# Kernel tuning notes

Hardware: AMD Instinct MI355X
Metric: run time of the kernel (lower is better)

Reference implementation:

```python
import jax, jax.numpy as jnp
import numpy as np

HEAD_DIM = 64
AGGR = 4  # attn_aggr_ratio
BN_EPS = 1e-5


def _conv1x1(x, W, b=None):
    # x: [N, Cin, L], W: [Cout, Cin] -> [N, Cout, L]
    y = jnp.einsum('ncl,oc->nol', x, W)
    if b is not None:
        y = y + b[None, :, None]
    return y


def _bn(x, gamma, beta, mean, var):
    # BatchNorm1d, eval mode (running stats). x: [N, C, L]
    inv = gamma * jax.lax.rsqrt(var + BN_EPS)
    return x * inv[None, :, None] + (beta - mean * inv)[None, :, None]


def setup_inputs() -> dict:
    key = jax.random.key(0)
    ks = jax.random.split(key, 8)
    N, C, L = 4, 256, 4096
    s = 1.0 / np.sqrt(C)
    inp = {
        'x': jax.random.normal(ks[0], (N, C, L), jnp.float32),
        'Wq': jax.random.normal(ks[1], (C, C), jnp.float32) * s,
        'bq': jnp.zeros((C,), jnp.float32),
        'Wk': jax.random.normal(ks[2], (C, C), jnp.float32) * s,
        'bk': jnp.zeros((C,), jnp.float32),
        'Wv': jax.random.normal(ks[3], (C, C), jnp.float32) * s,
        'bv': jnp.zeros((C,), jnp.float32),
        'Wo': jax.random.normal(ks[4], (C, C), jnp.float32) * s,
        'bo': jnp.zeros((C,), jnp.float32),
        'Wa': jax.random.normal(ks[5], (C, C), jnp.float32) * s,
        'g1': jnp.ones((C,), jnp.float32), 'b1': jnp.zeros((C,), jnp.float32),
        'm1': jnp.zeros((C,), jnp.float32), 'v1': jnp.ones((C,), jnp.float32),
        'g2': jnp.ones((C,), jnp.float32), 'b2': jnp.zeros((C,), jnp.float32),
        'm2': jnp.zeros((C,), jnp.float32), 'v2': jnp.ones((C,), jnp.float32),
    }
    return inp


def reference(x, Wq, bq, Wk, bk, Wv, bv, Wo, bo, Wa,
              g1, b1, m1, v1, g2, b2, m2, v2):
    N, C, L = x.shape
    H, E = C // HEAD_DIM, HEAD_DIM
    # q projection on full-resolution input
    q = _conv1x1(x, Wq, bq).reshape(N, H, E, L)
    # LocalAwareAggregationBlock: avg+max pool (kernel=AGGR, L divisible), 1x1 conv, BN
    xp = x.reshape(N, C, L // AGGR, AGGR)
    xa = xp.mean(axis=-1) + xp.max(axis=-1)          # [N, C, L//AGGR]
    xa = _conv1x1(xa, Wa)                             # bias=False
    xa = _bn(xa, g1, b1, m1, v1)
    # post-aggregation norm
    xa = _bn(xa, g2, b2, m2, v2)
    k = _conv1x1(xa, Wk, bk).reshape(N, H, E, -1)     # [N, H, E, L2]
    v = _conv1x1(xa, Wv, bv).reshape(N, H, E, -1)
    # attention: softmax((q/sqrt(E))^T k) @ v^T
    scale = 1.0 / np.sqrt(E)
    scores = jnp.einsum('nhel,nhem->nhlm', q * scale, k)  # [N, H, L, L2]
    attn = jax.nn.softmax(scores, axis=-1)
    o = jnp.einsum('nhlm,nhem->nhel', attn, v).reshape(N, C, L)
    return _conv1x1(o, Wo, bo)
```

## Files before the change

kernel.cpp:

```cpp
#include <hip/hip_runtime.h>
#include <stdint.h>

constexpr int NBATCH = 4;
constexpr int CH     = 256;
constexpr int LEN    = 4096;
constexpr int LPOOL  = 1024;
constexpr int NH     = 4;
constexpr int HD     = 64;

typedef __attribute__((ext_vector_type(8))) short short8;
typedef __attribute__((ext_vector_type(4))) float float4e;

__device__ __forceinline__ unsigned short f2bf(float f) {
    union { unsigned int i; float f; } v; v.f = f;
    unsigned int lsb = (v.i >> 16) & 1u;
    v.i += 0x7fffu + lsb;
    return (unsigned short)(v.i >> 16);
}
__device__ __forceinline__ unsigned pack2bf(float lo, float hi) {
    unsigned a = __float_as_uint(lo) + 0x8000u;
    unsigned b = __float_as_uint(hi) + 0x8000u;
    return __builtin_amdgcn_perm(b, a, 0x07060302u);
}

__global__ __launch_bounds__(256) void transpool_setup(
    const float* __restrict__ x, unsigned short* __restrict__ xbf,
    unsigned short* __restrict__ poolT,
    const float* __restrict__ w0, const float* __restrict__ w1,
    const float* __restrict__ w2, const float* __restrict__ w3,
    const float* __restrict__ w4, unsigned short* __restrict__ outW,
    const float* __restrict__ g1, const float* __restrict__ b1,
    const float* __restrict__ m1, const float* __restrict__ v1,
    const float* __restrict__ g2, const float* __restrict__ b2,
    const float* __restrict__ m2, const float* __restrict__ v2,
    float* __restrict__ scale, float* __restrict__ shift,
    const float* __restrict__ bk, const float* __restrict__ bv,
    float* __restrict__ bkv)
{
    __shared__ float T[64][65];
    __shared__ float P16[64][17];
    int b = blockIdx.x, t = threadIdx.x;
    if (b >= 1024) {
        int sb = b - 1024;
        if (sb < 320) {
            int gid = sb * 256 + t;
            int w = gid >> 14;
            int off = (gid & 16383) * 4;
            const float* src = (w == 0) ? w0 : (w == 1) ? w1 : (w == 2) ? w2 : (w == 3) ? w3 : w4;
            float4 v = *(const float4*)(src + off);
            uint2 pk;
            pk.x = pack2bf(v.x, v.y);
            pk.y = pack2bf(v.z, v.w);
            *(uint2*)(outW + w * 65536 + off) = pk;
        } else {
            float inv1 = g1[t] * rsqrtf(v1[t] + 1e-5f);
            float inv2 = g2[t] * rsqrtf(v2[t] + 1e-5f);
            scale[t] = inv1 * inv2;
            shift[t] = (b1[t] - m1[t] * inv1) * inv2 + (b2[t] - m2[t] * inv2);
            bkv[t] = bk[t];
            bkv[256 + t] = bv[t];
        }
        return;
    }
    int n = b >> 8, c0 = ((b >> 6) & 3) * 64, l0 = (b & 63) * 64;
    const float* xp = x + ((size_t)n * CH + c0) * LEN + l0;
    #pragma unroll
    for (int i = 0; i < 4; i++) {
        int idx = t + i * 256;
        int c = idx >> 4, l4 = idx & 15;
        float4 v = *(const float4*)(xp + (size_t)c * LEN + l4 * 4);
        T[c][l4 * 4 + 0] = v.x; T[c][l4 * 4 + 1] = v.y;
        T[c][l4 * 4 + 2] = v.z; T[c][l4 * 4 + 3] = v.w;
        P16[c][l4] = (v.x + v.y + v.z + v.w) * 0.25f
                   + fmaxf(fmaxf(v.x, v.y), fmaxf(v.z, v.w));
    }
    __syncthreads();
    unsigned short* op = xbf + ((size_t)n * LEN + l0) * CH + c0;
    #pragma unroll
    for (int i = 0; i < 4; i++) {
        int idx = t + i * 256;
        int l = idx >> 4, c4 = idx & 15;
        uint2 pk;
        pk.x = pack2bf(T[c4 * 4 + 0][l], T[c4 * 4 + 1][l]);
        pk.y = pack2bf(T[c4 * 4 + 2][l], T[c4 * 4 + 3][l]);
        *(uint2*)(op + (size_t)l * CH + c4 * 4) = pk;
    }
    int p0 = l0 >> 2;
    #pragma unroll
    for (int k = 0; k < 2; k++) {
        int p = (t >> 5) + k * 8;
        int c2 = (t & 31) * 2;
        unsigned pk = pack2bf(P16[c2][p], P16[c2 + 1][p]);
        *(unsigned*)(poolT + ((size_t)n * LPOOL + p0 + p) * CH + c0 + c2) = pk;
    }
}

__global__ __launch_bounds__(256) void gemm_mfma(
    const unsigned short* __restrict__ A,
    const unsigned short* __restrict__ B, size_t bBatch,
    const float* __restrict__ biasRow,
    const float* __restrict__ scale, const float* __restrict__ shift,
    float* __restrict__ outF, size_t oFBatch,
    unsigned short* __restrict__ out1, size_t o1Batch, int cs1,
    unsigned short* __restrict__ out2, size_t o2Batch, int rs2, int rowSplit,
    int NN, float outScale)
{
    __shared__ unsigned short smem[2 * 128 * 72];
    unsigned short* As = smem;
    unsigned short* Bs = smem + 128 * 72;

    int n = blockIdx.z;
    int t = threadIdx.x;
    int wave = t >> 6, lane = t & 63, m = lane & 15, quad = lane >> 4;
    int wm = wave & 1, wn = wave >> 1;
    int rowTile = blockIdx.y * 128;
    int col0 = blockIdx.x * 128;

    const unsigned short* Ab = A + (size_t)rowTile * 256;
    const unsigned short* Bb = B + (size_t)n * bBatch + (size_t)col0 * 256;

    float4e acc[4][4] = {};

    for (int kk = 0; kk < 256; kk += 64) {
        #pragma unroll
        for (int i = 0; i < 4; i++) {
            int idx = t + i * 256;
            int row = idx >> 3, ch = idx & 7;
            *(uint4*)&As[row * 72 + ch * 8] = *(const uint4*)(Ab + (size_t)row * 256 + kk + ch * 8);
            *(uint4*)&Bs[row * 72 + ch * 8] = *(const uint4*)(Bb + (size_t)row * 256 + kk + ch * 8);
        }
        __syncthreads();
        #pragma unroll
        for (int kc = 0; kc < 2; kc++) {
            short8 af[4], bfr[4];
            #pragma unroll
            for (int i = 0; i < 4; i++)
                af[i] = *(const short8*)&As[(wm * 64 + i * 16 + m) * 72 + kc * 32 + quad * 8];
            #pragma unroll
            for (int j = 0; j < 4; j++)
                bfr[j] = *(const short8*)&Bs[(wn * 64 + j * 16 + m) * 72 + kc * 32 + quad * 8];
            #pragma unroll
            for (int i = 0; i < 4; i++)
                #pragma unroll
                for (int j = 0; j < 4; j++)
                    acc[i][j] = __builtin_amdgcn_mfma_f32_16x16x32_bf16(af[i], bfr[j], acc[i][j], 0, 0, 0);
        }
        __syncthreads();
    }

    if (outF) {
        float* TOf = (float*)smem;
        float* dst = outF + (size_t)n * oFBatch;
        #pragma unroll
        for (int half = 0; half < 2; half++) {
            __syncthreads();
            if (wm == half) {
                #pragma unroll
                for (int i = 0; i < 4; i++) {
                    int rowL = i * 16 + quad * 4;
                    int rowG = rowTile + half * 64 + rowL;
                    float br[4], sc[4], sh[4];
                    #pragma unroll
                    for (int r = 0; r < 4; r++) {
                        br[r] = biasRow ? biasRow[rowG + r] : 0.0f;
                        sc[r] = scale ? scale[rowG + r] : 1.0f;
                        sh[r] = shift ? shift[rowG + r] : 0.0f;
                    }
                    #pragma unroll
                    for (int j = 0; j < 4; j++) {
                        int colL = wn * 64 + j * 16 + m;
                        float4e c = acc[i][j];
                        #pragma unroll
                        for (int r = 0; r < 4; r++)
                            TOf[(rowL + r) * 128 + colL] = ((c[r] + br[r]) * sc[r] + sh[r]) * outScale;
                    }
                }
            }
            __syncthreads();
            #pragma unroll
            for (int w = 0; w < 8; w++) {
                int idx = t + w * 256;
                int row = idx >> 5, c4 = idx & 31;
                *(float4*)(dst + (size_t)(rowTile + half * 64 + row) * NN + col0 + c4 * 4) =
                    *(const float4*)&TOf[row * 128 + c4 * 4];
            }
        }
        return;
    }

    bool mode2 = (rowTile >= rowSplit);
    unsigned short* TO = smem;
    #pragma unroll
    for (int i = 0; i < 4; i++) {
        int rowL = wm * 64 + i * 16 + quad * 4;
        int rowG = rowTile + rowL;
        float br[4], sc[4], sh[4];
        #pragma unroll
        for (int r = 0; r < 4; r++) {
            br[r] = biasRow ? biasRow[rowG + r] : 0.0f;
            sc[r] = scale ? scale[rowG + r] : 1.0f;
            sh[r] = shift ? shift[rowG + r] : 0.0f;
        }
        #pragma unroll
        for (int j = 0; j < 4; j++) {
            int colL = wn * 64 + j * 16 + m;
            float4e c = acc[i][j];
            float v0 = ((c[0] + br[0]) * sc[0] + sh[0]) * outScale;
            float v1 = ((c[1] + br[1]) * sc[1] + sh[1]) * outScale;
            float v2 = ((c[2] + br[2]) * sc[2] + sh[2]) * outScale;
            float v3 = ((c[3] + br[3]) * sc[3] + sh[3]) * outScale;
            if (!mode2) {
                uint2 pk;
                pk.x = pack2bf(v0, v1);
                pk.y = pack2bf(v2, v3);
                *(uint2*)&TO[colL * 136 + rowL] = pk;
            } else {
                TO[(rowL + 0) * 136 + colL] = f2bf(v0);
                TO[(rowL + 1) * 136 + colL] = f2bf(v1);
                TO[(rowL + 2) * 136 + colL] = f2bf(v2);
                TO[(rowL + 3) * 136 + colL] = f2bf(v3);
            }
        }
    }
    __syncthreads();
    if (!mode2) {
        unsigned short* dst = out1 + (size_t)n * o1Batch;
        #pragma unroll
        for (int w = 0; w < 8; w++) {
            int idx = t + w * 256;
            int l = idx >> 4, ch = idx & 15;
            *(uint4*)(dst + (size_t)(col0 + l) * cs1 + rowTile + ch * 8) =
                *(const uint4*)&TO[l * 136 + ch * 8];
        }
    } else {
        unsigned short* dst = out2 + (size_t)n * o2Batch;
        int rowBase = rowTile - rowSplit;
        #pragma unroll
        for (int w = 0; w < 8; w++) {
            int idx = t + w * 256;
            int row = idx >> 4, ch = idx & 15;
            *(uint4*)(dst + (size_t)(rowBase + row) * rs2 + col0 + ch * 8) =
                *(const uint4*)&TO[row * 136 + ch * 8];
        }
    }
}

__global__ __launch_bounds__(256, 4) void attn_mfma(
    const unsigned short* __restrict__ Qb,
    const unsigned short* __restrict__ Kb,
    const unsigned short* __restrict__ Vb,
    unsigned short* __restrict__ Obf)
{
    __shared__ unsigned short Ks[2][64 * 72];
    __shared__ unsigned short Vs[2][64 * 72];

    int qb = blockIdx.x;
    int h  = blockIdx.y;
    int n  = blockIdx.z;
    int t  = threadIdx.x;
    int wave = t >> 6, lane = t & 63;
    int m = lane & 15, quad = lane >> 4;
    int l0 = qb * 64 + wave * 16;

    const unsigned short* qp = Qb + ((size_t)n * LEN + l0 + m) * CH + h * HD + quad * 8;
    short8 bQ[2];
    bQ[0] = *(const short8*)qp;
    bQ[1] = *(const short8*)(qp + 32);

    float4e Oa[4] = {};
    float l_run = 0.0f;

    const unsigned short* KgBase = Kb + (size_t)n * LPOOL * CH + h * HD;
    const unsigned short* VgBase = Vb + ((size_t)n * CH + h * HD) * LPOOL;
    const float NEG = -17.312340f;

    int srow[2], sch[2];
    #pragma unroll
    for (int i = 0; i < 2; i++) {
        int idx = t + i * 256;
        srow[i] = idx >> 3; sch[i] = idx & 7;
    }

    uint4 kreg[2], vreg[2];
    #pragma unroll
    for (int i = 0; i < 2; i++) {
        kreg[i] = *(const uint4*)(KgBase + (size_t)srow[i] * CH + sch[i] * 8);
        vreg[i] = *(const uint4*)(VgBase + (size_t)srow[i] * LPOOL + sch[i] * 8);
    }
    #pragma unroll
    for (int i = 0; i < 2; i++) {
        *(uint4*)&Ks[0][srow[i] * 72 + sch[i] * 8] = kreg[i];
        *(uint4*)&Vs[0][srow[i] * 72 + sch[i] * 8] = vreg[i];
    }
    __syncthreads();

    for (int kt = 0; kt < 16; kt++) {
        int cur = kt & 1;
        if (kt < 15) {
            const unsigned short* Kg2 = KgBase + (size_t)(kt + 1) * 64 * CH;
            const unsigned short* Vg2 = VgBase + (kt + 1) * 64;
            #pragma unroll
            for (int i = 0; i < 2; i++) {
                kreg[i] = *(const uint4*)(Kg2 + (size_t)srow[i] * CH + sch[i] * 8);
                vreg[i] = *(const uint4*)(Vg2 + (size_t)srow[i] * LPOOL + sch[i] * 8);
            }
        }

        #pragma unroll
        for (int ch2 = 0; ch2 < 2; ch2++) {
            const unsigned short* kpE = &Ks[cur][(ch2 * 32 + m) * 72 + quad * 8];
            const unsigned short* kpO = kpE + 16 * 72;
            short8 aE0 = *(const short8*)kpE;
            short8 aE1 = *(const short8*)(kpE + 32);
            short8 aO0 = *(const short8*)kpO;
            short8 aO1 = *(const short8*)(kpO + 32);
            union { unsigned u[4]; short8 s; } aV[4];
            #pragma unroll
            for (int eb = 0; eb < 4; eb++) {
                const unsigned short* vp = &Vs[cur][(eb * 16 + m) * 72 + ch2 * 32 + quad * 4];
                *(uint2*)&aV[eb].u[0] = *(const uint2*)vp;
                *(uint2*)&aV[eb].u[2] = *(const uint2*)(vp + 16);
            }

            float4e cE = {NEG, NEG, NEG, NEG};
            cE = __builtin_amdgcn_mfma_f32_16x16x32_bf16(aE0, bQ[0], cE, 0, 0, 0);
            cE = __builtin_amdgcn_mfma_f32_16x16x32_bf16(aE1, bQ[1], cE, 0, 0, 0);
            float4e cO = {NEG, NEG, NEG, NEG};
            cO = __builtin_amdgcn_mfma_f32_16x16x32_bf16(aO0, bQ[0], cO, 0, 0, 0);
            cO = __builtin_amdgcn_mfma_f32_16x16x32_bf16(aO1, bQ[1], cO, 0, 0, 0);
            float pE0 = exp2f(cE[0]), pE1 = exp2f(cE[1]);
            float pE2 = exp2f(cE[2]), pE3 = exp2f(cE[3]);
            float pO0 = exp2f(cO[0]), pO1 = exp2f(cO[1]);
            float pO2 = exp2f(cO[2]), pO3 = exp2f(cO[3]);
            l_run += ((pE0 + pE1) + (pE2 + pE3)) + ((pO0 + pO1) + (pO2 + pO3));
            union { unsigned u[4]; short8 s; } bP;
            bP.u[0] = pack2bf(pE0, pE1);
            bP.u[1] = pack2bf(pE2, pE3);
            bP.u[2] = pack2bf(pO0, pO1);
            bP.u[3] = pack2bf(pO2, pO3);
            #pragma unroll
            for (int eb = 0; eb < 4; eb++)
                Oa[eb] = __builtin_amdgcn_mfma_f32_16x16x32_bf16(aV[eb].s, bP.s, Oa[eb], 0, 0, 0);
        }

        if (kt < 15) {
            int nxt = cur ^ 1;
            #pragma unroll
            for (int i = 0; i < 2; i++) {
                *(uint4*)&Ks[nxt][srow[i] * 72 + sch[i] * 8] = kreg[i];
                *(uint4*)&Vs[nxt][srow[i] * 72 + sch[i] * 8] = vreg[i];
            }
            __syncthreads();
        }
    }

    {
        float l = l_run;
        l += __shfl_xor(l, 16);
        l += __shfl_xor(l, 32);
        float inv = 1.0f / l;
        unsigned short* op = Obf + ((size_t)n * LEN + l0 + m) * CH + h * HD;
        #pragma unroll
        for (int eb = 0; eb < 4; eb++) {
            uint2 pk;
            pk.x = pack2bf(Oa[eb][0] * inv, Oa[eb][1] * inv);
            pk.y = pack2bf(Oa[eb][2] * inv, Oa[eb][3] * inv);
            *(uint2*)(op + eb * 16 + quad * 4) = pk;
        }
    }
}

extern "C" void kernel_launch(void* const* d_in, const int* in_sizes, int n_in,
                              void* d_out, int out_size, void* d_ws, size_t ws_size,
                              hipStream_t stream)
{
    const float* x  = (const float*)d_in[0];
    const float* Wq = (const float*)d_in[1];
    const float* bq = (const float*)d_in[2];
    const float* Wk = (const float*)d_in[3];
    const float* bk = (const float*)d_in[4];
    const float* Wv = (const float*)d_in[5];
    const float* bv = (const float*)d_in[6];
    const float* Wo = (const float*)d_in[7];
    const float* bo = (const float*)d_in[8];
    const float* Wa = (const float*)d_in[9];
    const float* g1 = (const float*)d_in[10];
    const float* b1 = (const float*)d_in[11];
    const float* m1 = (const float*)d_in[12];
    const float* v1 = (const float*)d_in[13];
    const float* g2 = (const float*)d_in[14];
    const float* b2 = (const float*)d_in[15];
    const float* m2 = (const float*)d_in[16];
    const float* v2 = (const float*)d_in[17];

    float* wsf      = (float*)d_ws;
    float* bn_scale = wsf;
    float* bn_shift = wsf + 256;
    float* bkv      = wsf + 512;
    unsigned short* Wbf   = (unsigned short*)(wsf + 1024);
    unsigned short* xbf   = Wbf + 5 * 65536;
    unsigned short* poolT = xbf   + (size_t)NBATCH * LEN * CH;
    unsigned short* xabf  = poolT + (size_t)NBATCH * LPOOL * CH;
    unsigned short* Kbf   = xabf  + (size_t)NBATCH * LPOOL * CH;
    unsigned short* Vbf   = Kbf   + (size_t)NBATCH * LPOOL * CH;
    unsigned short* Qbf   = Vbf   + (size_t)NBATCH * LPOOL * CH;
    unsigned short* Obf   = Qbf   + (size_t)NBATCH * LEN * CH;

    transpool_setup<<<1345, 256, 0, stream>>>(x, xbf, poolT,
        Wq, Wk, Wv, Wo, Wa, Wbf,
        g1, b1, m1, v1, g2, b2, m2, v2, bn_scale, bn_shift, bk, bv, bkv);

    gemm_mfma<<<dim3(32, 2, 4), 256, 0, stream>>>(
        Wbf + 0 * 65536, xbf, (size_t)LEN * CH, bq, nullptr, nullptr,
        nullptr, 0, Qbf, (size_t)LEN * CH, 256, nullptr, 0, 0, 1 << 30,
        LEN, 0.18033688f);

    gemm_mfma<<<dim3(8, 2, 4), 256, 0, stream>>>(
        Wbf + 4 * 65536, poolT, (size_t)LPOOL * CH, nullptr, bn_scale, bn_shift,
        nullptr, 0, xabf, (size_t)LPOOL * CH, 256, nullptr, 0, 0, 1 << 30,
        LPOOL, 1.0f);

    gemm_mfma<<<dim3(8, 4, 4), 256, 0, stream>>>(
        Wbf + 1 * 65536, xabf, (size_t)LPOOL * CH, bkv, nullptr, nullptr,
        nullptr, 0, Kbf, (size_t)LPOOL * CH, 256, Vbf, (size_t)LPOOL * CH, LPOOL, 256,
        LPOOL, 1.0f);

    attn_mfma<<<dim3(LEN / 64, NH, NBATCH), 256, 0, stream>>>(Qbf, Kbf, Vbf, Obf);

    gemm_mfma<<<dim3(32, 2, 4), 256, 0, stream>>>(
        Wbf + 3 * 65536, Obf, (size_t)LEN * CH, bo, nullptr, nullptr,
        (float*)d_out, (size_t)CH * LEN, nullptr, 0, 0, nullptr, 0, 0, 1 << 30,
        LEN, 1.0f);
}
```

Measured before the change: 178.5 us.

## Switch attention kernel to 32x32x16 MFMA with swizzled LDS and permlane swaps

Rewrites the attention inner loop to use 32x32x16 bf16 MFMA tiles, with each wave handling 32 query rows, so a block now covers 128 queries and the grid is halved. The padded LDS layout is replaced by an XOR-swizzled 64-column layout to avoid bank conflicts. P is redistributed into B-operand layout with permlane32_swap instead of being re-read. The aim is fewer MFMA issues and fewer LDS reads per unit of work, traded against more registers per thread (occupancy hint lowered to 2) and fewer blocks to fill the GPU.

```diff
diff --git a/kernel.cpp b/kernel.cpp
--- a/kernel.cpp
+++ b/kernel.cpp
@@ -10,6 +10,8 @@
 
 typedef __attribute__((ext_vector_type(8))) short short8;
 typedef __attribute__((ext_vector_type(4))) float float4e;
+typedef __attribute__((ext_vector_type(16))) float float16e;
+typedef __attribute__((ext_vector_type(2))) unsigned uint2v;
 
 __device__ __forceinline__ unsigned short f2bf(float f) {
     union { unsigned int i; float f; } v; v.f = f;
@@ -245,41 +247,56 @@
     }
 }
 
-__global__ __launch_bounds__(256, 4) void attn_mfma(
+__global__ __launch_bounds__(256, 2) void attn_mfma(
     const unsigned short* __restrict__ Qb,
     const unsigned short* __restrict__ Kb,
     const unsigned short* __restrict__ Vb,
     unsigned short* __restrict__ Obf)
 {
-    __shared__ unsigned short Ks[2][64 * 72];
-    __shared__ unsigned short Vs[2][64 * 72];
+    __shared__ unsigned short Ks[2][64 * 64];
+    __shared__ unsigned short Vs[2][64 * 64];
 
     int qb = blockIdx.x;
     int h  = blockIdx.y;
     int n  = blockIdx.z;
     int t  = threadIdx.x;
     int wave = t >> 6, lane = t & 63;
-    int m = lane & 15, quad = lane >> 4;
-    int l0 = qb * 64 + wave * 16;
-
-    const unsigned short* qp = Qb + ((size_t)n * LEN + l0 + m) * CH + h * HD + quad * 8;
-    short8 bQ[2];
-    bQ[0] = *(const short8*)qp;
-    bQ[1] = *(const short8*)(qp + 32);
-
-    float4e Oa[4] = {};
+    int col = lane & 31;
+    int hi  = lane >> 5;
+    int l0 = qb * 128 + wave * 32;
+
+    const unsigned short* qp = Qb + ((size_t)n * LEN + l0 + col) * CH + h * HD + hi * 8;
+    short8 bQ[4];
+    #pragma unroll
+    for (int dc = 0; dc < 4; dc++)
+        bQ[dc] = *(const short8*)(qp + dc * 16);
+
+    float16e Oa[2];
+    #pragma unroll
+    for (int e = 0; e < 2; e++)
+        #pragma unroll
+        for (int r = 0; r < 16; r++) Oa[e][r] = 0.0f;
     float l_run = 0.0f;
 
     const unsigned short* KgBase = Kb + (size_t)n * LPOOL * CH + h * HD;
     const unsigned short* VgBase = Vb + ((size_t)n * CH + h * HD) * LPOOL;
     const float NEG = -17.312340f;
 
-    int srow[2], sch[2];
+    int srow[2], sch[2], sdst[2];
     #pragma unroll
     for (int i = 0; i < 2; i++) {
         int idx = t + i * 256;
         srow[i] = idx >> 3; sch[i] = idx & 7;
-    }
+        sdst[i] = srow[i] * 128 + ((sch[i] * 16) ^ ((srow[i] & 7) << 4));
+    }
+    int ldoff[2][4];
+    #pragma unroll
+    for (int g = 0; g < 2; g++)
+        #pragma unroll
+        for (int c = 0; c < 4; c++) {
+            int row = g * 32 + col;
+            ldoff[g][c] = row * 128 + ((c * 32 + hi * 16) ^ ((row & 7) << 4));
+        }
 
     uint4 kreg[2], vreg[2];
     #pragma unroll
@@ -289,8 +306,8 @@
     }
     #pragma unroll
     for (int i = 0; i < 2; i++) {
-        *(uint4*)&Ks[0][srow[i] * 72 + sch[i] * 8] = kreg[i];
-        *(uint4*)&Vs[0][srow[i] * 72 + sch[i] * 8] = vreg[i];
+        *(uint4*)((char*)Ks[0] + sdst[i]) = kreg[i];
+        *(uint4*)((char*)Vs[0] + sdst[i]) = vreg[i];
     }
     __syncthreads();
 
@@ -306,68 +323,71 @@
             }
         }
 
-        #pragma unroll
-        for (int ch2 = 0; ch2 < 2; ch2++) {
-            const unsigned short* kpE = &Ks[cur][(ch2 * 32 + m) * 72 + quad * 8];
-            const unsigned short* kpO = kpE + 16 * 72;
-            short8 aE0 = *(const short8*)kpE;
-            short8 aE1 = *(const short8*)(kpE + 32);
-            short8 aO0 = *(const short8*)kpO;
-            short8 aO1 = *(const short8*)(kpO + 32);
-            union { unsigned u[4]; short8 s; } aV[4];
-            #pragma unroll
-            for (int eb = 0; eb < 4; eb++) {
-                const unsigned short* vp = &Vs[cur][(eb * 16 + m) * 72 + ch2 * 32 + quad * 4];
-                *(uint2*)&aV[eb].u[0] = *(const uint2*)vp;
-                *(uint2*)&aV[eb].u[2] = *(const uint2*)(vp + 16);
-            }
-
-            float4e cE = {NEG, NEG, NEG, NEG};
-            cE = __builtin_amdgcn_mfma_f32_16x16x32_bf16(aE0, bQ[0], cE, 0, 0, 0);
-            cE = __builtin_amdgcn_mfma_f32_16x16x32_bf16(aE1, bQ[1], cE, 0, 0, 0);
-            float4e cO = {NEG, NEG, NEG, NEG};
-            cO = __builtin_amdgcn_mfma_f32_16x16x32_bf16(aO0, bQ[0], cO, 0, 0, 0);
-            cO = __builtin_amdgcn_mfma_f32_16x16x32_bf16(aO1, bQ[1], cO, 0, 0, 0);
-            float pE0 = exp2f(cE[0]), pE1 = exp2f(cE[1]);
-            float pE2 = exp2f(cE[2]), pE3 = exp2f(cE[3]);
-            float pO0 = exp2f(cO[0]), pO1 = exp2f(cO[1]);
-            float pO2 = exp2f(cO[2]), pO3 = exp2f(cO[3]);
-            l_run += ((pE0 + pE1) + (pE2 + pE3)) + ((pO0 + pO1) + (pO2 + pO3));
-            union { unsigned u[4]; short8 s; } bP;
-            bP.u[0] = pack2bf(pE0, pE1);
-            bP.u[1] = pack2bf(pE2, pE3);
-            bP.u[2] = pack2bf(pO0, pO1);
-            bP.u[3] = pack2bf(pO2, pO3);
-            #pragma unroll
-            for (int eb = 0; eb < 4; eb++)
-                Oa[eb] = __builtin_amdgcn_mfma_f32_16x16x32_bf16(aV[eb].s, bP.s, Oa[eb], 0, 0, 0);
+        const char* KsC = (const char*)Ks[cur];
+        const char* VsC = (const char*)Vs[cur];
+        #pragma unroll
+        for (int kh = 0; kh < 2; kh++) {
+            float16e c;
+            #pragma unroll
+            for (int r = 0; r < 16; r++) c[r] = NEG;
+            #pragma unroll
+            for (int dc = 0; dc < 4; dc++) {
+                short8 a = *(const short8*)(KsC + ldoff[kh][dc]);
+                c = __builtin_amdgcn_mfma_f32_32x32x16_bf16(a, bQ[dc], c, 0, 0, 0);
+            }
+            float p[16];
+            #pragma unroll
+            for (int r = 0; r < 16; r++) p[r] = exp2f(c[r]);
+            l_run += ((p[0] + p[1]) + (p[2] + p[3])) + ((p[4] + p[5]) + (p[6] + p[7]))
+                   + ((p[8] + p[9]) + (p[10] + p[11])) + ((p[12] + p[13]) + (p[14] + p[15]));
+            union { unsigned u[4]; short8 s; } bP[2];
+            #pragma unroll
+            for (int kc2 = 0; kc2 < 2; kc2++) {
+                int rb = kc2 * 8;
+                unsigned A0 = pack2bf(p[rb + 0], p[rb + 1]);
+                unsigned B0 = pack2bf(p[rb + 4], p[rb + 5]);
+                unsigned A1 = pack2bf(p[rb + 2], p[rb + 3]);
+                unsigned B1 = pack2bf(p[rb + 6], p[rb + 7]);
+                uint2v s0 = __builtin_amdgcn_permlane32_swap(A0, B0, false, false);
+                uint2v s1 = __builtin_amdgcn_permlane32_swap(A1, B1, false, false);
+                bP[kc2].u[0] = s0[0];
+                bP[kc2].u[1] = s1[0];
+                bP[kc2].u[2] = s0[1];
+                bP[kc2].u[3] = s1[1];
+            }
+            #pragma unroll
+            for (int eh = 0; eh < 2; eh++)
+                #pragma unroll
+                for (int kc2 = 0; kc2 < 2; kc2++) {
+                    short8 av = *(const short8*)(VsC + ldoff[eh][kh * 2 + kc2]);
+                    Oa[eh] = __builtin_amdgcn_mfma_f32_32x32x16_bf16(av, bP[kc2].s, Oa[eh], 0, 0, 0);
+                }
         }
 
         if (kt < 15) {
             int nxt = cur ^ 1;
             #pragma unroll
             for (int i = 0; i < 2; i++) {
-                *(uint4*)&Ks[nxt][srow[i] * 72 + sch[i] * 8] = kreg[i];
-                *(uint4*)&Vs[nxt][srow[i] * 72 + sch[i] * 8] = vreg[i];
+                *(uint4*)((char*)Ks[nxt] + sdst[i]) = kreg[i];
+                *(uint4*)((char*)Vs[nxt] + sdst[i]) = vreg[i];
             }
             __syncthreads();
         }
     }
 
-    {
-        float l = l_run;
-        l += __shfl_xor(l, 16);
-        l += __shfl_xor(l, 32);
-        float inv = 1.0f / l;
-        unsigned short* op = Obf + ((size_t)n * LEN + l0 + m) * CH + h * HD;
-        #pragma unroll
-        for (int eb = 0; eb < 4; eb++) {
+    float l = l_run + __shfl_xor(l_run, 32);
+    float inv = 1.0f / l;
+    unsigned short* op = Obf + ((size_t)n * LEN + l0 + col) * CH + h * HD + hi * 4;
+    #pragma unroll
+    for (int eh = 0; eh < 2; eh++)
+        #pragma unroll
+        for (int rq = 0; rq < 4; rq++) {
+            int r = rq * 4;
             uint2 pk;
-            pk.x = pack2bf(Oa[eb][0] * inv, Oa[eb][1] * inv);
-            pk.y = pack2bf(Oa[eb][2] * inv, Oa[eb][3] * inv);
-            *(uint2*)(op + eb * 16 + quad * 4) = pk;
-        }
-    }
+            pk.x = pack2bf(Oa[eh][r + 0] * inv, Oa[eh][r + 1] * inv);
+            pk.y = pack2bf(Oa[eh][r + 2] * inv, Oa[eh][r + 3] * inv);
+            *(uint2*)(op + eh * 32 + rq * 8) = pk;
+        }
 }
 
 extern "C" void kernel_launch(void* const* d_in, const int* in_sizes, int n_in,
@@ -425,7 +445,7 @@
         nullptr, 0, Kbf, (size_t)LPOOL * CH, 256, Vbf, (size_t)LPOOL * CH, LPOOL, 256,
         LPOOL, 1.0f);
 
-    attn_mfma<<<dim3(LEN / 64, NH, NBATCH), 256, 0, stream>>>(Qbf, Kbf, Vbf, Obf);
+    attn_mfma<<<dim3(LEN / 128, NH, NBATCH), 256, 0, stream>>>(Qbf, Kbf, Vbf, Obf);
 
     gemm_mfma<<<dim3(32, 2, 4), 256, 0, stream>>>(
         Wbf + 3 * 65536, Obf, (size_t)LEN * CH, bo, nullptr, nullptr,
```

Result: no change. 181.6 us (+1.7%).
